# Kernel optimization log

Measured on AMD Instinct MI355X. Metric: run time of the kernel, lower is better.

The kernel has to match this reference:

```python
import jax, jax.numpy as jnp
from jax import lax
import numpy as np

N = 10000   # nodes
E = 160000  # edges (avg degree 16)
C = 64      # in_channels / out_channels
T = 12      # input time steps
H = 64      # hidden_channels (must be 64 for GReTo psi broadcast)
TS = T - 2  # tlen_spconv after first causal conv (k=3, no padding)
F = H * TS  # GCN feature dim = 640

def _conv1d(x, w, b):
    # x: [N, Cin, T], w: [Cout, Cin, K] -> [N, Cout, T-K+1] (causal, no padding)
    out = lax.conv_general_dilated(x, w, window_strides=(1,), padding='VALID',
                                   dimension_numbers=('NCH', 'OIH', 'NCH'))
    return out + b[None, :, None]

def _time_conv(x, w1, b1, w2, b2):
    # gated TCN: tanh(conv1) * sigmoid(conv2)
    return jnp.tanh(_conv1d(x, w1, b1)) * jax.nn.sigmoid(_conv1d(x, w2, b2))

def _gcn(x, W, b, src, dst, ew, n):
    # PyG GCNConv: add self-loops (weight 1.0), symmetric normalization, x@W, scatter-sum, +bias
    loop = jnp.arange(n)
    s = jnp.concatenate([src, loop])
    d = jnp.concatenate([dst, loop])
    w = jnp.concatenate([ew, jnp.ones((n,), ew.dtype)])
    deg = jax.ops.segment_sum(w, d, num_segments=n)
    dis = jnp.where(deg > 0, deg ** -0.5, 0.0)
    norm = dis[s] * w * dis[d]                 # [E+N]
    h = x @ W                                  # [n, F]
    out = jax.ops.segment_sum(norm[:, None] * h[s], d, num_segments=n)
    return out + b

def setup_inputs():
    key = jax.random.key(0)
    ks = jax.random.split(key, 16)
    s = 0.05
    return {
        'x': jax.random.normal(ks[0], (N, C, T), jnp.float32),
        'edge_index': jax.random.randint(ks[1], (2, E), 0, N),
        'edge_attr': jax.random.uniform(ks[2], (E, 2), dtype=jnp.float32),
        'ND_t': jax.random.normal(ks[3], (N, 3), jnp.float32),
        'tc1_w1': jax.random.normal(ks[4], (H, C, 3), jnp.float32) * s,
        'tc1_b1': jnp.zeros((H,), jnp.float32),
        'tc1_w2': jax.random.normal(ks[5], (H, C, 3), jnp.float32) * s,
        'tc1_b2': jnp.zeros((H,), jnp.float32),
        'W_pos': jax.random.normal(ks[6], (F, F), jnp.float32) * s,
        'b_pos': jnp.zeros((F,), jnp.float32),
        'W_neg': jax.random.normal(ks[7], (F, F), jnp.float32) * s,
        'b_neg': jnp.zeros((F,), jnp.float32),
        'gre_W': jax.random.normal(ks[8], (2 * H, H), jnp.float32) * s,
        'gre_b': jnp.zeros((H,), jnp.float32),
        'psi_W1': jax.random.normal(ks[9], (3, 64), jnp.float32) * s,
        'psi_b1': jnp.zeros((64,), jnp.float32),
        'psi_W2': jax.random.normal(ks[10], (64, 3), jnp.float32) * s,
        'psi_b2': jnp.zeros((3,), jnp.float32),
        'tc2_w1': jax.random.normal(ks[11], (C, H, 3), jnp.float32) * s,
        'tc2_b1': jnp.zeros((C,), jnp.float32),
        'tc2_w2': jax.random.normal(ks[12], (C, H, 3), jnp.float32) * s,
        'tc2_b2': jnp.zeros((C,), jnp.float32),
    }

def reference(x, edge_index, edge_attr, ND_t,
              tc1_w1, tc1_b1, tc1_w2, tc1_b2,
              W_pos, b_pos, W_neg, b_neg, gre_W, gre_b,
              psi_W1, psi_b1, psi_W2, psi_b2,
              tc2_w1, tc2_b1, tc2_w2, tc2_b2):
    n = x.shape[0]
    out1 = _time_conv(x, tc1_w1, tc1_b1, tc1_w2, tc1_b2)   # [N, H, TS]
    d0, d1, d2 = out1.shape
    src, dst = edge_index[0], edge_index[1]
    w_pos = edge_attr[:, 0] + 1.0
    w_neg = edge_attr[:, 1] + 1.0
    # psi: [N, 3] -> one scalar per node per hop; repeat_interleave in torch is
    # just a broadcast since psi is constant over the H and TS dims
    psi = jax.nn.relu(ND_t @ psi_W1 + psi_b1) @ psi_W2 + psi_b2
    out0 = out1.reshape(d0, -1)                             # [N, H*TS]
    cur = out0
    acc = jnp.zeros((d0, d1, d2), x.dtype)
    for i in range(3):  # k = 3 positive-graph hops
        h = jax.nn.relu(_gcn(cur, W_pos, b_pos, src, dst, w_pos, n).reshape(d0, d1, d2))
        acc = acc + psi[:, i][:, None, None] * h
        cur = h.reshape(d0, -1)
    out_neg = jax.nn.relu(_gcn(out0, W_neg, b_neg, src, dst, w_neg, n).reshape(d0, d1, d2))
    out2 = jnp.concatenate([acc, out_neg], axis=1)          # [N, 2H, TS]
    out2 = jax.nn.relu(jnp.einsum('nct,cd->ndt', out2, gre_W) + gre_b[None, :, None])
    out3 = _time_conv(out2, tc2_w1, tc2_b1, tc2_w2, tc2_b2) # [N, C, TS-2]
    return out3
```

## Files before the change

kernel.cpp:

```cpp
#include <hip/hip_runtime.h>
#include <math.h>

#define NN   10000
#define NE   160000
#define CCH  64
#define TIN  12
#define HCH  64
#define TSP  10
#define FF   640
#define TOUT 8
#define NR   (NN * TSP)
#define NR2  (NN * TOUT)


typedef _Float16 f16;
typedef _Float16 f16x4 __attribute__((ext_vector_type(4)));
typedef _Float16 f16x8 __attribute__((ext_vector_type(8)));
typedef float f32x4 __attribute__((ext_vector_type(4)));

#define GLD_LDS(gsrc, ldst) __builtin_amdgcn_global_load_lds( \
    (const __attribute__((address_space(1))) void*)(gsrc),    \
    (__attribute__((address_space(3))) void*)(ldst), 16, 0, 0)

__global__ __launch_bounds__(256) void k_xT(const float* __restrict__ x, f16* __restrict__ xT)
{
    __shared__ float xs[4][CCH * TIN];
    int node0 = blockIdx.x * 4;
    for (int i = threadIdx.x; i < 4 * CCH * TIN; i += 256) {
        int nn = i / (CCH * TIN), off = i % (CCH * TIN);
        int g = node0 + nn;
        xs[nn][off] = (g < NN) ? x[(size_t)g * CCH * TIN + off] : 0.f;
    }
    __syncthreads();
    for (int i = threadIdx.x; i < 4 * CCH * TIN; i += 256) {
        int nn = i / (CCH * TIN), off = i % (CCH * TIN);
        int t = off >> 6, c = off & 63;
        int g = node0 + nn;
        if (g < NN) xT[(size_t)g * (CCH * TIN) + off] = (f16)xs[nn][c * TIN + t];
    }
}

__global__ void k_wconv2(const float* __restrict__ w1a, const float* __restrict__ w2a,
                         const float* __restrict__ w1b, const float* __restrict__ w2b,
                         f16* __restrict__ d1, f16* __restrict__ d2)
{
    int tid = blockIdx.x * 256 + threadIdx.x;
    const int half = 128 * 192;
    if (tid >= 2 * half) return;
    int which = tid / half, r = tid % half;
    const float* s1 = which ? w1b : w1a;
    const float* s2 = which ? w2b : w2a;
    f16* dst = which ? d2 : d1;
    int o = r / 192, j = r % 192;
    int k = j >> 6, ci = j & 63;
    const float* src = (o < 64) ? s1 : s2;
    dst[r] = (f16)src[((o & 63) * 64 + ci) * 3 + k];
}

__global__ __launch_bounds__(256) void k_tcn1g(const f16* __restrict__ A,
                                               const f16* __restrict__ Bw,
                                               const float* __restrict__ b1,
                                               const float* __restrict__ b2,
                                               f16* __restrict__ out)
{
    __shared__ f16 Bs[128][200];
    int tid = threadIdx.x;
#pragma unroll
    for (int i = 0; i < 12; ++i) {
        int c = tid + i * 256;
        int row = c / 24, seg = (c % 24) * 8;
        *(f16x8*)&Bs[row][seg] = *(const f16x8*)&Bw[row * 192 + seg];
    }
    __syncthreads();

    int w = tid >> 6, l = tid & 63;
    int row0 = blockIdx.x * 128 + w * 32;
    int lrow = l & 15, lk = (l >> 4) * 8;

    size_t abase[2];
#pragma unroll
    for (int m = 0; m < 2; ++m) {
        int rr = row0 + m * 16 + lrow;
        int rc = (rr < NR) ? rr : NR - 1;
        int n = rc / 10, t = rc - n * 10;
        abase[m] = (size_t)n * 768 + t * 64 + lk;
    }
    f32x4 acc[2][8];
#pragma unroll
    for (int m = 0; m < 2; ++m)
#pragma unroll
        for (int n = 0; n < 8; ++n)
            acc[m][n] = (f32x4){0.f, 0.f, 0.f, 0.f};

#pragma unroll
    for (int ks = 0; ks < 6; ++ks) {
        f16x8 af[2], bf[8];
#pragma unroll
        for (int m = 0; m < 2; ++m)
            af[m] = *(const f16x8*)&A[abase[m] + ks * 32];
#pragma unroll
        for (int n = 0; n < 8; ++n)
            bf[n] = *(const f16x8*)&Bs[n * 16 + lrow][ks * 32 + lk];
#pragma unroll
        for (int m = 0; m < 2; ++m)
#pragma unroll
            for (int n = 0; n < 8; ++n)
                acc[m][n] = __builtin_amdgcn_mfma_f32_16x16x32_f16(af[m], bf[n], acc[m][n], 0, 0, 0);
    }
    int og = (l >> 4) * 4;
#pragma unroll
    for (int m = 0; m < 2; ++m) {
#pragma unroll
        for (int n = 0; n < 4; ++n) {
            int h = n * 16 + lrow;
            float bb1 = b1[h], bb2 = b2[h];
#pragma unroll
            for (int rr = 0; rr < 4; ++rr) {
                int R = row0 + m * 16 + og + rr;
                if (R < NR) {
                    float g1 = acc[m][n][rr] + bb1;
                    float g2 = acc[m][n + 4][rr] + bb2;
                    float e = __expf(2.f * g1);
                    float th = 1.f - 2.f / (e + 1.f);
                    float sg = 1.f / (1.f + __expf(-g2));
                    out[(size_t)R * 64 + h] = (f16)(th * sg);
                }
            }
        }
    }
}

__global__ __launch_bounds__(256) void k_tcn2g(const f16* __restrict__ A,
                                               const f16* __restrict__ Bw,
                                               const float* __restrict__ b1,
                                               const float* __restrict__ b2,
                                               float* __restrict__ out)
{
    __shared__ f16 Bs[128][200];
    int tid = threadIdx.x;
#pragma unroll
    for (int i = 0; i < 12; ++i) {
        int c = tid + i * 256;
        int row = c / 24, seg = (c % 24) * 8;
        *(f16x8*)&Bs[row][seg] = *(const f16x8*)&Bw[row * 192 + seg];
    }
    __syncthreads();

    int w = tid >> 6, l = tid & 63;
    int row0 = blockIdx.x * 128 + w * 32;
    int lrow = l & 15, lk = (l >> 4) * 8;

    size_t abase[2];
#pragma unroll
    for (int m = 0; m < 2; ++m) {
        int rr = row0 + m * 16 + lrow;
        int rc = (rr < NR2) ? rr : NR2 - 1;
        int n = rc >> 3, t = rc & 7;
        abase[m] = (size_t)n * FF + t * 64 + lk;
    }
    f32x4 acc[2][8];
#pragma unroll
    for (int m = 0; m < 2; ++m)
#pragma unroll
        for (int n = 0; n < 8; ++n)
            acc[m][n] = (f32x4){0.f, 0.f, 0.f, 0.f};

#pragma unroll
    for (int ks = 0; ks < 6; ++ks) {
        f16x8 af[2], bf[8];
#pragma unroll
        for (int m = 0; m < 2; ++m)
            af[m] = *(const f16x8*)&A[abase[m] + ks * 32];
#pragma unroll
        for (int n = 0; n < 8; ++n)
            bf[n] = *(const f16x8*)&Bs[n * 16 + lrow][ks * 32 + lk];
#pragma unroll
        for (int m = 0; m < 2; ++m)
#pragma unroll
            for (int n = 0; n < 8; ++n)
                acc[m][n] = __builtin_amdgcn_mfma_f32_16x16x32_f16(af[m], bf[n], acc[m][n], 0, 0, 0);
    }
    int og = (l >> 4) * 4;
#pragma unroll
    for (int m = 0; m < 2; ++m) {
#pragma unroll
        for (int n = 0; n < 4; ++n) {
            int c = n * 16 + lrow;
            float bb1 = b1[c], bb2 = b2[c];
#pragma unroll
            for (int rr = 0; rr < 4; ++rr) {
                int R = row0 + m * 16 + og + rr;
                if (R < NR2) {
                    float g1 = acc[m][n][rr] + bb1;
                    float g2 = acc[m][n + 4][rr] + bb2;
                    float e = __expf(2.f * g1);
                    float th = 1.f - 2.f / (e + 1.f);
                    float sg = 1.f / (1.f + __expf(-g2));
                    int n2 = R >> 3, t2 = R & 7;
                    out[(size_t)n2 * (CCH * TOUT) + c * TOUT + t2] = th * sg;
                }
            }
        }
    }
}

__global__ void k_psi(const float* __restrict__ ND, const float* __restrict__ W1,
                      const float* __restrict__ b1, const float* __restrict__ W2,
                      const float* __restrict__ b2, float* __restrict__ psi)
{
    int n = blockIdx.x * blockDim.x + threadIdx.x;
    if (n >= NN) return;
    float d0 = ND[n * 3], d1 = ND[n * 3 + 1], d2 = ND[n * 3 + 2];
    float o0 = b2[0], o1 = b2[1], o2 = b2[2];
    for (int j = 0; j < 64; ++j) {
        float hv = d0 * W1[j] + d1 * W1[64 + j] + d2 * W1[128 + j] + b1[j];
        hv = fmaxf(hv, 0.f);
        o0 += hv * W2[j * 3 + 0];
        o1 += hv * W2[j * 3 + 1];
        o2 += hv * W2[j * 3 + 2];
    }
    psi[n * 3 + 0] = o0; psi[n * 3 + 1] = o1; psi[n * 3 + 2] = o2;
}

__global__ void k_deg(const int* __restrict__ ei, const float* __restrict__ ea,
                      int* __restrict__ cnt, float* __restrict__ degp, float* __restrict__ degn)
{
    int e = blockIdx.x * blockDim.x + threadIdx.x;
    if (e >= NE) return;
    int d = ei[NE + e];
    atomicAdd(&cnt[d], 1);
    atomicAdd(&degp[d], ea[e * 2 + 0] + 1.f);
    atomicAdd(&degn[d], ea[e * 2 + 1] + 1.f);
}

__global__ void k_dis(const float* __restrict__ degp, const float* __restrict__ degn,
                      float* __restrict__ disp, float* __restrict__ disn)
{
    int n = blockIdx.x * blockDim.x + threadIdx.x;
    if (n >= NN) return;
    disp[n] = 1.f / sqrtf(degp[n] + 1.f);
    disn[n] = 1.f / sqrtf(degn[n] + 1.f);
}

__global__ __launch_bounds__(1024) void k_scan(const int* __restrict__ cnt, int* __restrict__ rowptr)
{
    __shared__ int buf[1024];
    __shared__ int carry;
    if (threadIdx.x == 0) carry = 0;
    __syncthreads();
    for (int base = 0; base < NN; base += 1024) {
        int i = base + threadIdx.x;
        int v = (i < NN) ? cnt[i] : 0;
        buf[threadIdx.x] = v;
        __syncthreads();
        for (int off = 1; off < 1024; off <<= 1) {
            int t = (threadIdx.x >= (unsigned)off) ? buf[threadIdx.x - off] : 0;
            __syncthreads();
            buf[threadIdx.x] += t;
            __syncthreads();
        }
        if (i < NN) rowptr[i] = carry + buf[threadIdx.x] - v;
        __syncthreads();
        if (threadIdx.x == 0) carry += buf[1023];
        __syncthreads();
    }
    if (threadIdx.x == 0) rowptr[NN] = carry;
}

__global__ void k_fill(const int* __restrict__ ei, const float* __restrict__ ea,
                       const int* __restrict__ rowptr, int* __restrict__ cursor,
                       const float* __restrict__ disp, const float* __restrict__ disn,
                       int* __restrict__ colsrc, float* __restrict__ normp, float* __restrict__ normn)
{
    int e = blockIdx.x * blockDim.x + threadIdx.x;
    if (e >= NE) return;
    int s = ei[e], d = ei[NE + e];
    int slot = atomicAdd(&cursor[d], 1);
    int idx = rowptr[d] + slot;
    colsrc[idx] = s;
    normp[idx] = disp[s] * (ea[e * 2 + 0] + 1.f) * disp[d];
    normn[idx] = disn[s] * (ea[e * 2 + 1] + 1.f) * disn[d];
}

__global__ __launch_bounds__(256) void k_wsplit2(const float* __restrict__ Wa,
                                                 const float* __restrict__ Wb,
                                                 f16* __restrict__ Wt)
{
    __shared__ float t[32][33];
    const float* W = blockIdx.z ? Wb : Wa;
    f16* dst = Wt + (size_t)blockIdx.z * FF * FF;
    int bx = blockIdx.x * 32;
    int by = blockIdx.y * 32;
    int tx = threadIdx.x & 31, ty = threadIdx.x >> 5;
#pragma unroll
    for (int j = 0; j < 4; ++j)
        t[ty + j * 8][tx] = W[(size_t)(bx + ty + j * 8) * 640 + by + tx];
    __syncthreads();
#pragma unroll
    for (int j = 0; j < 4; ++j)
        dst[(size_t)(by + ty + j * 8) * 640 + bx + tx] = (f16)t[tx][ty + j * 8];
}

__global__ __launch_bounds__(640) void k_perm2(const f16* __restrict__ Wt0,
                                               f16* __restrict__ Wp, f16* __restrict__ Wn)
{
    __shared__ f16 row[FF];
    const f16* src = Wt0 + (size_t)blockIdx.z * FF * FF;
    f16* dst = blockIdx.z ? Wn : Wp;
    int np = blockIdx.x;
    int n = (np & 63) * 10 + (np >> 6);
    int tid = threadIdx.x;
    row[tid] = src[(size_t)n * FF + tid];
    __syncthreads();
    int k = (tid & 63) * 10 + (tid >> 6);
    dst[(size_t)np * FF + tid] = row[k];
}

__global__ void k_gwt(const float* __restrict__ gW, f16* __restrict__ gWt)
{
    int tid = blockIdx.x * 256 + threadIdx.x;
    if (tid >= 128 * 64) return;
    int c = tid >> 6, d = tid & 63;
    gWt[d * 128 + c] = (f16)gW[tid];
}

__global__ __launch_bounds__(256) void k_gemm16(const f16* __restrict__ A,
                                                const f16* __restrict__ Bt,
                                                f16* __restrict__ C, int M)
{
    __shared__ f16 As[128 * 32];
    __shared__ f16 Bs[64 * 32];
    int tid = threadIdx.x;
    int row0 = blockIdx.y * 128;
    int col0 = blockIdx.x * 64;
    int w = tid >> 6, l = tid & 63;
    int wr = (w >> 1) * 64;
    int wc = (w & 1) * 32;
    int lrow = l & 15;
    int lk = (l >> 4) * 8;

    int arow = w * 32 + (l >> 2);
    int brow = w * 16 + (l >> 2);
    int seg  = (l & 3) * 8;

    f32x4 acc[4][2];
#pragma unroll
    for (int m = 0; m < 4; ++m)
#pragma unroll
        for (int n = 0; n < 2; ++n)
            acc[m][n] = (f32x4){0.f, 0.f, 0.f, 0.f};

    for (int k0 = 0; k0 < FF; k0 += 32) {
        __syncthreads();
        GLD_LDS(&A[(size_t)(row0 + arow) * FF + k0 + seg],       &As[w * 1024]);
        GLD_LDS(&A[(size_t)(row0 + arow + 16) * FF + k0 + seg],  &As[w * 1024 + 512]);
        GLD_LDS(&Bt[(size_t)(col0 + brow) * FF + k0 + seg],      &Bs[w * 512]);
        __syncthreads();
        f16x8 af[4], bf[2];
#pragma unroll
        for (int m = 0; m < 4; ++m)
            af[m] = *(const f16x8*)&As[(wr + m * 16 + lrow) * 32 + lk];
#pragma unroll
        for (int n = 0; n < 2; ++n)
            bf[n] = *(const f16x8*)&Bs[(wc + n * 16 + lrow) * 32 + lk];
#pragma unroll
        for (int m = 0; m < 4; ++m)
#pragma unroll
            for (int n = 0; n < 2; ++n)
                acc[m][n] = __builtin_amdgcn_mfma_f32_16x16x32_f16(af[m], bf[n], acc[m][n], 0, 0, 0);
    }
    int orow = (l >> 4) * 4;
#pragma unroll
    for (int m = 0; m < 4; ++m) {
#pragma unroll
        for (int r = 0; r < 4; ++r) {
            int rr = row0 + wr + m * 16 + orow + r;
            if (rr < M) {
#pragma unroll
                for (int n = 0; n < 2; ++n)
                    C[(size_t)rr * FF + col0 + wc + n * 16 + lrow] = (f16)acc[m][n][r];
            }
        }
    }
}

__global__ __launch_bounds__(192) void k_agg(const f16* __restrict__ hsrc,
                      const int* __restrict__ rowptr, const int* __restrict__ colsrc,
                      const float* __restrict__ enorm, const float* __restrict__ dis,
                      const float* __restrict__ bias, f16* __restrict__ hout)
{
    __shared__ int   s_idx[128];
    __shared__ float s_w[128];
    int d = blockIdx.x;
    int lane = threadIdx.x;
    int c0 = lane * 4;
    bool act = lane < 160;
    float v0 = 0.f, v1 = 0.f, v2 = 0.f, v3 = 0.f;
    if (act) {
        float selfw = dis[d] * dis[d];
        f16x4 self = *(const f16x4*)&hsrc[(size_t)d * FF + c0];
        v0 = selfw * (float)self[0];
        v1 = selfw * (float)self[1];
        v2 = selfw * (float)self[2];
        v3 = selfw * (float)self[3];
    }
    int beg = rowptr[d], end = rowptr[d + 1];
    for (int base = beg; base < end; base += 128) {
        int cnt = (end - base < 128) ? (end - base) : 128;
        __syncthreads();
        for (int j = lane; j < cnt; j += 192) {
            s_idx[j] = colsrc[base + j];
            s_w[j]   = enorm[base + j];
        }
        __syncthreads();
        if (act) {
            for (int i = 0; i < cnt; ++i) {
                f16x4 p = *(const f16x4*)&hsrc[(size_t)s_idx[i] * FF + c0];
                float w = s_w[i];
                v0 += w * (float)p[0];
                v1 += w * (float)p[1];
                v2 += w * (float)p[2];
                v3 += w * (float)p[3];
            }
        }
    }
    if (act) {
        f16x4 o;
        float vv[4] = {v0, v1, v2, v3};
#pragma unroll
        for (int j = 0; j < 4; ++j) {
            int c = c0 + j;
            o[j] = (f16)fmaxf(vv[j] + bias[(c & 63) * 10 + (c >> 6)], 0.f);
        }
        *(f16x4*)&hout[(size_t)d * FF + c0] = o;
    }
}

__global__ __launch_bounds__(256) void k_greto2(const f16* __restrict__ h1,
                        const f16* __restrict__ h2, const f16* __restrict__ h3,
                        const f16* __restrict__ hneg, const float* __restrict__ psi,
                        const f16* __restrict__ gWt, const float* __restrict__ gb,
                        f16* __restrict__ out)
{
    __shared__ f16 As[128][132];
    __shared__ f16 Bs[64][132];
    int tid = threadIdx.x;
    int row0 = blockIdx.x * 128;

    for (int cb = tid; cb < 1024; cb += 256) {
        int d = cb >> 4, seg = (cb & 15) * 8;
        *(f16x8*)&Bs[d][seg] = *(const f16x8*)&gWt[d * 128 + seg];
    }
    int lr = tid >> 1, side = tid & 1;
    int r = row0 + lr;
    if (r < NR) {
        int n = r / 10, t = r - (r / 10) * 10;
        size_t base = (size_t)n * FF + t * 64;
        if (side == 0) {
            float p0 = psi[n * 3], p1 = psi[n * 3 + 1], p2 = psi[n * 3 + 2];
#pragma unroll
            for (int i = 0; i < 8; ++i) {
                f16x8 a = *(const f16x8*)&h1[base + i * 8];
                f16x8 b = *(const f16x8*)&h2[base + i * 8];
                f16x8 c = *(const f16x8*)&h3[base + i * 8];
                f16x8 o;
#pragma unroll
                for (int j = 0; j < 8; ++j)
                    o[j] = (f16)(p0 * (float)a[j] + p1 * (float)b[j] + p2 * (float)c[j]);
                *(f16x8*)&As[lr][i * 8] = o;
            }
        } else {
#pragma unroll
            for (int i = 0; i < 8; ++i)
                *(f16x8*)&As[lr][64 + i * 8] = *(const f16x8*)&hneg[base + i * 8];
        }
    } else {
        f16x8 z = {};
#pragma unroll
        for (int i = 0; i < 8; ++i)
            *(f16x8*)&As[lr][side * 64 + i * 8] = z;
    }
    __syncthreads();

    int w = tid >> 6, l = tid & 63;
    int wr = w * 32;
    int lrow = l & 15;
    int lk = (l >> 4) * 8;
    f32x4 acc[2][4];
#pragma unroll
    for (int m = 0; m < 2; ++m)
#pragma unroll
        for (int n = 0; n < 4; ++n)
            acc[m][n] = (f32x4){0.f, 0.f, 0.f, 0.f};
#pragma unroll
    for (int ks = 0; ks < 4; ++ks) {
        f16x8 af[2], bf[4];
#pragma unroll
        for (int m = 0; m < 2; ++m)
            af[m] = *(const f16x8*)&As[wr + m * 16 + lrow][ks * 32 + lk];
#pragma unroll
        for (int n = 0; n < 4; ++n)
            bf[n] = *(const f16x8*)&Bs[n * 16 + lrow][ks * 32 + lk];
#pragma unroll
        for (int m = 0; m < 2; ++m)
#pragma unroll
            for (int n = 0; n < 4; ++n)
                acc[m][n] = __builtin_amdgcn_mfma_f32_16x16x32_f16(af[m], bf[n], acc[m][n], 0, 0, 0);
    }
    int orow = (l >> 4) * 4;
#pragma unroll
    for (int m = 0; m < 2; ++m) {
#pragma unroll
        for (int rr = 0; rr < 4; ++rr) {
            int ro = row0 + wr + m * 16 + orow + rr;
            if (ro < NR) {
#pragma unroll
                for (int n = 0; n < 4; ++n) {
                    int col = n * 16 + lrow;
                    out[(size_t)ro * 64 + col] = (f16)fmaxf(acc[m][n][rr] + gb[col], 0.f);
                }
            }
        }
    }
}

extern "C" void kernel_launch(void* const* d_in, const int* in_sizes, int n_in,
                              void* d_out, int out_size, void* d_ws, size_t ws_size,
                              hipStream_t stream)
{
    const float* x     = (const float*)d_in[0];
    const int*   ei    = (const int*)  d_in[1];
    const float* ea    = (const float*)d_in[2];
    const float* ndt   = (const float*)d_in[3];
    const float* tc1w1 = (const float*)d_in[4];
    const float* tc1b1 = (const float*)d_in[5];
    const float* tc1w2 = (const float*)d_in[6];
    const float* tc1b2 = (const float*)d_in[7];
    const float* Wpos  = (const float*)d_in[8];
    const float* bpos  = (const float*)d_in[9];
    const float* Wneg  = (const float*)d_in[10];
    const float* bneg  = (const float*)d_in[11];
    const float* greW  = (const float*)d_in[12];
    const float* greb  = (const float*)d_in[13];
    const float* psiW1 = (const float*)d_in[14];
    const float* psib1 = (const float*)d_in[15];
    const float* psiW2 = (const float*)d_in[16];
    const float* psib2 = (const float*)d_in[17];
    const float* tc2w1 = (const float*)d_in[18];
    const float* tc2b1 = (const float*)d_in[19];
    const float* tc2w2 = (const float*)d_in[20];
    const float* tc2b2 = (const float*)d_in[21];
    float* out = (float*)d_out;

    char* p = (char*)d_ws;
    int*   cnt   = (int*)p;   p += (size_t)NN * 4;
    int*   cursor= (int*)p;   p += (size_t)NN * 4;
    float* degp  = (float*)p; p += (size_t)NN * 4;
    float* degn  = (float*)p; p += (size_t)NN * 4;
    f16*   xT    = (f16*)p;   p += (size_t)NN * CCH * TIN * 2;
    f16*   out0h = (f16*)p;   p += (size_t)NN * FF * 2;
    f16*   h1    = (f16*)p;   p += (size_t)NN * FF * 2;
    f16*   h2    = (f16*)p;   p += (size_t)NN * FF * 2;
    f16*   h3    = (f16*)p;   p += (size_t)NN * FF * 2;
    f16*   hneg  = (f16*)p;   p += (size_t)NN * FF * 2;
    f16*   Cb16  = (f16*)p;   p += (size_t)NN * FF * 2;
    f16*   Gbuf  = (f16*)p;   p += (size_t)NN * FF * 2;
    f16*   Wtp   = (f16*)p;   p += (size_t)FF * FF * 2;
    f16*   Wtn   = (f16*)p;   p += (size_t)FF * FF * 2;
    f16*   Wtmp  = (f16*)p;   p += (size_t)2 * FF * FF * 2;
    f16*   gWt   = (f16*)p;   p += (size_t)128 * 64 * 2;
    f16*   Bw1   = (f16*)p;   p += (size_t)128 * 192 * 2;
    f16*   Bw2   = (f16*)p;   p += (size_t)128 * 192 * 2;
    float* psib  = (float*)p; p += (size_t)NN * 3 * 4;
    float* disp  = (float*)p; p += (size_t)NN * 4;
    float* disn  = (float*)p; p += (size_t)NN * 4;
    float* normp = (float*)p; p += (size_t)NE * 4;
    float* normn = (float*)p; p += (size_t)NE * 4;
    int* rowptr  = (int*)p;   p += (size_t)(NN + 1) * 4;
    int* colsrc  = (int*)p;   p += (size_t)NE * 4;

    (void)hipMemsetAsync(cnt, 0, (size_t)4 * NN * 4, stream);

    k_xT<<<2500, 256, 0, stream>>>(x, xT);
    k_wconv2<<<(2 * 128 * 192 + 255) / 256, 256, 0, stream>>>(tc1w1, tc1w2, tc2w1, tc2w2, Bw1, Bw2);
    k_tcn1g<<<(NR + 127) / 128, 256, 0, stream>>>(xT, Bw1, tc1b1, tc1b2, out0h);
    k_psi<<<(NN + 255) / 256, 256, 0, stream>>>(ndt, psiW1, psib1, psiW2, psib2, psib);
    k_deg<<<(NE + 255) / 256, 256, 0, stream>>>(ei, ea, cnt, degp, degn);
    k_dis<<<(NN + 255) / 256, 256, 0, stream>>>(degp, degn, disp, disn);
    k_scan<<<1, 1024, 0, stream>>>(cnt, rowptr);
    k_fill<<<(NE + 255) / 256, 256, 0, stream>>>(ei, ea, rowptr, cursor, disp, disn,
                                                 colsrc, normp, normn);
    dim3 wgrid(20, 20, 2);
    k_wsplit2<<<wgrid, 256, 0, stream>>>(Wpos, Wneg, Wtmp);
    dim3 pgrid(FF, 1, 2);
    k_perm2<<<pgrid, 640, 0, stream>>>(Wtmp, Wtp, Wtn);
    k_gwt<<<(128 * 64 + 255) / 256, 256, 0, stream>>>(greW, gWt);

    dim3 ggrid(FF / 64, (NN + 127) / 128);
    k_gemm16<<<ggrid, 256, 0, stream>>>(out0h, Wtp, Cb16, NN);
    k_agg<<<NN, 192, 0, stream>>>(Cb16, rowptr, colsrc, normp, disp, bpos, h1);
    k_gemm16<<<ggrid, 256, 0, stream>>>(h1, Wtp, Cb16, NN);
    k_agg<<<NN, 192, 0, stream>>>(Cb16, rowptr, colsrc, normp, disp, bpos, h2);
    k_gemm16<<<ggrid, 256, 0, stream>>>(h2, Wtp, Cb16, NN);
    k_agg<<<NN, 192, 0, stream>>>(Cb16, rowptr, colsrc, normp, disp, bpos, h3);
    k_gemm16<<<ggrid, 256, 0, stream>>>(out0h, Wtn, Cb16, NN);
    k_agg<<<NN, 192, 0, stream>>>(Cb16, rowptr, colsrc, normn, disn, bneg, hneg);
    k_greto2<<<(NR + 127) / 128, 256, 0, stream>>>(h1, h2, h3, hneg, psib, gWt, greb, Gbuf);
    k_tcn2g<<<(NR2 + 127) / 128, 256, 0, stream>>>(Gbuf, Bw2, tc2b1, tc2b2, out);
}
```

Before: 397.2 us.

## Merge preprocessing kernels, parallelize scan, widen aggregation to 8-wide vectors

Folds the x transpose, conv weight conversion, psi MLP, GReTo weight transpose, degree counting and W split-transpose into one block-indexed prep kernel. This cuts the number of launches. The degree-inverse-sqrt step moves into the scan kernel, and the scan becomes a single pass where each thread sums 10 counts before one block-wide prefix sum. The GCN aggregation kernel now uses 128 threads with 8-element f16 vector loads per lane instead of 192 threads with 4-element loads, which halves the gather instructions per neighbor row but leaves fewer active lanes per node.

```diff
diff --git a/kernel.cpp b/kernel.cpp
--- a/kernel.cpp
+++ b/kernel.cpp
@@ -12,9 +12,7 @@
 #define NR   (NN * TSP)
 #define NR2  (NN * TOUT)
 
-
 typedef _Float16 f16;
-typedef _Float16 f16x4 __attribute__((ext_vector_type(4)));
 typedef _Float16 f16x8 __attribute__((ext_vector_type(8)));
 typedef float f32x4 __attribute__((ext_vector_type(4)));
 
@@ -22,39 +20,104 @@
     (const __attribute__((address_space(1))) void*)(gsrc),    \
     (__attribute__((address_space(3))) void*)(ldst), 16, 0, 0)
 
-__global__ __launch_bounds__(256) void k_xT(const float* __restrict__ x, f16* __restrict__ xT)
-{
-    __shared__ float xs[4][CCH * TIN];
-    int node0 = blockIdx.x * 4;
-    for (int i = threadIdx.x; i < 4 * CCH * TIN; i += 256) {
-        int nn = i / (CCH * TIN), off = i % (CCH * TIN);
-        int g = node0 + nn;
-        xs[nn][off] = (g < NN) ? x[(size_t)g * CCH * TIN + off] : 0.f;
-    }
-    __syncthreads();
-    for (int i = threadIdx.x; i < 4 * CCH * TIN; i += 256) {
-        int nn = i / (CCH * TIN), off = i % (CCH * TIN);
-        int t = off >> 6, c = off & 63;
-        int g = node0 + nn;
-        if (g < NN) xT[(size_t)g * (CCH * TIN) + off] = (f16)xs[nn][c * TIN + t];
-    }
-}
-
-__global__ void k_wconv2(const float* __restrict__ w1a, const float* __restrict__ w2a,
-                         const float* __restrict__ w1b, const float* __restrict__ w2b,
-                         f16* __restrict__ d1, f16* __restrict__ d2)
-{
-    int tid = blockIdx.x * 256 + threadIdx.x;
-    const int half = 128 * 192;
-    if (tid >= 2 * half) return;
-    int which = tid / half, r = tid % half;
-    const float* s1 = which ? w1b : w1a;
-    const float* s2 = which ? w2b : w2a;
-    f16* dst = which ? d2 : d1;
-    int o = r / 192, j = r % 192;
-    int k = j >> 6, ci = j & 63;
-    const float* src = (o < 64) ? s1 : s2;
-    dst[r] = (f16)src[((o & 63) * 64 + ci) * 3 + k];
+#define PB_XT   2500
+#define PB_WC   (PB_XT + 192)
+#define PB_PSI  (PB_WC + 40)
+#define PB_GWT  (PB_PSI + 32)
+#define PB_DEG  (PB_GWT + 625)
+#define PB_WS   (PB_DEG + 800)
+
+__global__ __launch_bounds__(256) void k_prep(
+    const float* __restrict__ x, f16* __restrict__ xT,
+    const float* __restrict__ tc1w1, const float* __restrict__ tc1w2,
+    const float* __restrict__ tc2w1, const float* __restrict__ tc2w2,
+    f16* __restrict__ Bw1, f16* __restrict__ Bw2,
+    const float* __restrict__ ND, const float* __restrict__ pW1,
+    const float* __restrict__ pb1, const float* __restrict__ pW2,
+    const float* __restrict__ pb2, float* __restrict__ psi,
+    const float* __restrict__ gW, f16* __restrict__ gWt,
+    const int* __restrict__ ei, const float* __restrict__ ea,
+    int* __restrict__ cnt, float* __restrict__ degp, float* __restrict__ degn,
+    const float* __restrict__ Wpos, const float* __restrict__ Wneg,
+    f16* __restrict__ Wtmp)
+{
+    __shared__ float smem[3072];
+    int blk = blockIdx.x;
+    int tid = threadIdx.x;
+
+    if (blk < PB_XT) {
+        float (*xs)[CCH * TIN] = (float(*)[CCH * TIN])smem;
+        int node0 = blk * 4;
+        for (int i = tid; i < 4 * CCH * TIN; i += 256) {
+            int nn = i / (CCH * TIN), off = i % (CCH * TIN);
+            int g = node0 + nn;
+            xs[nn][off] = (g < NN) ? x[(size_t)g * CCH * TIN + off] : 0.f;
+        }
+        __syncthreads();
+        for (int i = tid; i < 4 * CCH * TIN; i += 256) {
+            int nn = i / (CCH * TIN), off = i % (CCH * TIN);
+            int t = off >> 6, c = off & 63;
+            int g = node0 + nn;
+            if (g < NN) xT[(size_t)g * (CCH * TIN) + off] = (f16)xs[nn][c * TIN + t];
+        }
+    } else if (blk < PB_WC) {
+        int t2 = (blk - PB_XT) * 256 + tid;
+        const int half = 128 * 192;
+        if (t2 < 2 * half) {
+            int which = t2 / half, r = t2 % half;
+            const float* s1 = which ? tc2w1 : tc1w1;
+            const float* s2 = which ? tc2w2 : tc1w2;
+            f16* dst = which ? Bw2 : Bw1;
+            int o = r / 192, j = r % 192;
+            int k = j >> 6, ci = j & 63;
+            const float* src = (o < 64) ? s1 : s2;
+            dst[r] = (f16)src[((o & 63) * 64 + ci) * 3 + k];
+        }
+    } else if (blk < PB_PSI) {
+        int n = (blk - PB_WC) * 256 + tid;
+        if (n < NN) {
+            float d0 = ND[n * 3], d1 = ND[n * 3 + 1], d2 = ND[n * 3 + 2];
+            float o0 = pb2[0], o1 = pb2[1], o2 = pb2[2];
+            for (int j = 0; j < 64; ++j) {
+                float hv = d0 * pW1[j] + d1 * pW1[64 + j] + d2 * pW1[128 + j] + pb1[j];
+                hv = fmaxf(hv, 0.f);
+                o0 += hv * pW2[j * 3 + 0];
+                o1 += hv * pW2[j * 3 + 1];
+                o2 += hv * pW2[j * 3 + 2];
+            }
+            psi[n * 3 + 0] = o0; psi[n * 3 + 1] = o1; psi[n * 3 + 2] = o2;
+        }
+    } else if (blk < PB_GWT) {
+        int t2 = (blk - PB_PSI) * 256 + tid;
+        if (t2 < 128 * 64) {
+            int c = t2 >> 6, d = t2 & 63;
+            gWt[d * 128 + c] = (f16)gW[t2];
+        }
+    } else if (blk < PB_DEG) {
+        int e = (blk - PB_GWT) * 256 + tid;
+        if (e < NE) {
+            int d = ei[NE + e];
+            atomicAdd(&cnt[d], 1);
+            atomicAdd(&degp[d], ea[e * 2 + 0] + 1.f);
+            atomicAdd(&degn[d], ea[e * 2 + 1] + 1.f);
+        }
+    } else {
+        float (*tt)[33] = (float(*)[33])smem;
+        int rel = blk - PB_DEG;
+        int z = rel / 400, r2 = rel % 400;
+        const float* W = z ? Wneg : Wpos;
+        f16* dst = Wtmp + (size_t)z * FF * FF;
+        int bx = (r2 / 20) * 32;
+        int by = (r2 % 20) * 32;
+        int tx = tid & 31, ty = tid >> 5;
+#pragma unroll
+        for (int j = 0; j < 4; ++j)
+            tt[ty + j * 8][tx] = W[(size_t)(bx + ty + j * 8) * 640 + by + tx];
+        __syncthreads();
+#pragma unroll
+        for (int j = 0; j < 4; ++j)
+            dst[(size_t)(by + ty + j * 8) * 640 + bx + tx] = (f16)tt[tx][ty + j * 8];
+    }
 }
 
 __global__ __launch_bounds__(256) void k_tcn1g(const f16* __restrict__ A,
@@ -204,67 +267,38 @@
     }
 }
 
-__global__ void k_psi(const float* __restrict__ ND, const float* __restrict__ W1,
-                      const float* __restrict__ b1, const float* __restrict__ W2,
-                      const float* __restrict__ b2, float* __restrict__ psi)
-{
-    int n = blockIdx.x * blockDim.x + threadIdx.x;
-    if (n >= NN) return;
-    float d0 = ND[n * 3], d1 = ND[n * 3 + 1], d2 = ND[n * 3 + 2];
-    float o0 = b2[0], o1 = b2[1], o2 = b2[2];
-    for (int j = 0; j < 64; ++j) {
-        float hv = d0 * W1[j] + d1 * W1[64 + j] + d2 * W1[128 + j] + b1[j];
-        hv = fmaxf(hv, 0.f);
-        o0 += hv * W2[j * 3 + 0];
-        o1 += hv * W2[j * 3 + 1];
-        o2 += hv * W2[j * 3 + 2];
-    }
-    psi[n * 3 + 0] = o0; psi[n * 3 + 1] = o1; psi[n * 3 + 2] = o2;
-}
-
-__global__ void k_deg(const int* __restrict__ ei, const float* __restrict__ ea,
-                      int* __restrict__ cnt, float* __restrict__ degp, float* __restrict__ degn)
-{
-    int e = blockIdx.x * blockDim.x + threadIdx.x;
-    if (e >= NE) return;
-    int d = ei[NE + e];
-    atomicAdd(&cnt[d], 1);
-    atomicAdd(&degp[d], ea[e * 2 + 0] + 1.f);
-    atomicAdd(&degn[d], ea[e * 2 + 1] + 1.f);
-}
-
-__global__ void k_dis(const float* __restrict__ degp, const float* __restrict__ degn,
+__global__ __launch_bounds__(1024) void k_scan(const int* __restrict__ cnt,
+                      int* __restrict__ rowptr,
+                      const float* __restrict__ degp, const float* __restrict__ degn,
                       float* __restrict__ disp, float* __restrict__ disn)
 {
-    int n = blockIdx.x * blockDim.x + threadIdx.x;
-    if (n >= NN) return;
-    disp[n] = 1.f / sqrtf(degp[n] + 1.f);
-    disn[n] = 1.f / sqrtf(degn[n] + 1.f);
-}
-
-__global__ __launch_bounds__(1024) void k_scan(const int* __restrict__ cnt, int* __restrict__ rowptr)
-{
-    __shared__ int buf[1024];
-    __shared__ int carry;
-    if (threadIdx.x == 0) carry = 0;
+    int tid = threadIdx.x;
+    for (int i = tid; i < NN; i += 1024) {
+        disp[i] = 1.f / sqrtf(degp[i] + 1.f);
+        disn[i] = 1.f / sqrtf(degn[i] + 1.f);
+    }
+    __shared__ int part[1024];
+    int base = tid * 10;
+    int loc[10];
+    int sum = 0;
+    if (tid < 1000) {
+#pragma unroll
+        for (int j = 0; j < 10; ++j) { loc[j] = sum; sum += cnt[base + j]; }
+    }
+    part[tid] = (tid < 1000) ? sum : 0;
     __syncthreads();
-    for (int base = 0; base < NN; base += 1024) {
-        int i = base + threadIdx.x;
-        int v = (i < NN) ? cnt[i] : 0;
-        buf[threadIdx.x] = v;
-        __syncthreads();
-        for (int off = 1; off < 1024; off <<= 1) {
-            int t = (threadIdx.x >= (unsigned)off) ? buf[threadIdx.x - off] : 0;
-            __syncthreads();
-            buf[threadIdx.x] += t;
-            __syncthreads();
-        }
-        if (i < NN) rowptr[i] = carry + buf[threadIdx.x] - v;
-        __syncthreads();
-        if (threadIdx.x == 0) carry += buf[1023];
-        __syncthreads();
-    }
-    if (threadIdx.x == 0) rowptr[NN] = carry;
+    for (int off = 1; off < 1024; off <<= 1) {
+        int t = (tid >= off) ? part[tid - off] : 0;
+        __syncthreads();
+        part[tid] += t;
+        __syncthreads();
+    }
+    int prefix = (tid > 0) ? part[tid - 1] : 0;
+    if (tid < 1000) {
+#pragma unroll
+        for (int j = 0; j < 10; ++j) rowptr[base + j] = prefix + loc[j];
+    }
+    if (tid == 0) rowptr[NN] = part[1023];
 }
 
 __global__ void k_fill(const int* __restrict__ ei, const float* __restrict__ ea,
@@ -280,25 +314,6 @@
     colsrc[idx] = s;
     normp[idx] = disp[s] * (ea[e * 2 + 0] + 1.f) * disp[d];
     normn[idx] = disn[s] * (ea[e * 2 + 1] + 1.f) * disn[d];
-}
-
-__global__ __launch_bounds__(256) void k_wsplit2(const float* __restrict__ Wa,
-                                                 const float* __restrict__ Wb,
-                                                 f16* __restrict__ Wt)
-{
-    __shared__ float t[32][33];
-    const float* W = blockIdx.z ? Wb : Wa;
-    f16* dst = Wt + (size_t)blockIdx.z * FF * FF;
-    int bx = blockIdx.x * 32;
-    int by = blockIdx.y * 32;
-    int tx = threadIdx.x & 31, ty = threadIdx.x >> 5;
-#pragma unroll
-    for (int j = 0; j < 4; ++j)
-        t[ty + j * 8][tx] = W[(size_t)(bx + ty + j * 8) * 640 + by + tx];
-    __syncthreads();
-#pragma unroll
-    for (int j = 0; j < 4; ++j)
-        dst[(size_t)(by + ty + j * 8) * 640 + bx + tx] = (f16)t[tx][ty + j * 8];
 }
 
 __global__ __launch_bounds__(640) void k_perm2(const f16* __restrict__ Wt0,
@@ -316,14 +331,6 @@
     dst[(size_t)np * FF + tid] = row[k];
 }
 
-__global__ void k_gwt(const float* __restrict__ gW, f16* __restrict__ gWt)
-{
-    int tid = blockIdx.x * 256 + threadIdx.x;
-    if (tid >= 128 * 64) return;
-    int c = tid >> 6, d = tid & 63;
-    gWt[d * 128 + c] = (f16)gW[tid];
-}
-
 __global__ __launch_bounds__(256) void k_gemm16(const f16* __restrict__ A,
                                                 const f16* __restrict__ Bt,
                                                 f16* __restrict__ C, int M)
@@ -384,7 +391,7 @@
     }
 }
 
-__global__ __launch_bounds__(192) void k_agg(const f16* __restrict__ hsrc,
+__global__ __launch_bounds__(128) void k_agg(const f16* __restrict__ hsrc,
                       const int* __restrict__ rowptr, const int* __restrict__ colsrc,
                       const float* __restrict__ enorm, const float* __restrict__ dis,
                       const float* __restrict__ bias, f16* __restrict__ hout)
@@ -393,46 +400,41 @@
     __shared__ float s_w[128];
     int d = blockIdx.x;
     int lane = threadIdx.x;
-    int c0 = lane * 4;
-    bool act = lane < 160;
-    float v0 = 0.f, v1 = 0.f, v2 = 0.f, v3 = 0.f;
+    int c0 = lane * 8;
+    bool act = lane < 80;
+    float v[8] = {0.f, 0.f, 0.f, 0.f, 0.f, 0.f, 0.f, 0.f};
     if (act) {
         float selfw = dis[d] * dis[d];
-        f16x4 self = *(const f16x4*)&hsrc[(size_t)d * FF + c0];
-        v0 = selfw * (float)self[0];
-        v1 = selfw * (float)self[1];
-        v2 = selfw * (float)self[2];
-        v3 = selfw * (float)self[3];
+        f16x8 self = *(const f16x8*)&hsrc[(size_t)d * FF + c0];
+#pragma unroll
+        for (int j = 0; j < 8; ++j) v[j] = selfw * (float)self[j];
     }
     int beg = rowptr[d], end = rowptr[d + 1];
     for (int base = beg; base < end; base += 128) {
         int cnt = (end - base < 128) ? (end - base) : 128;
         __syncthreads();
-        for (int j = lane; j < cnt; j += 192) {
-            s_idx[j] = colsrc[base + j];
-            s_w[j]   = enorm[base + j];
+        if (lane < cnt) {
+            s_idx[lane] = colsrc[base + lane];
+            s_w[lane]   = enorm[base + lane];
         }
         __syncthreads();
         if (act) {
             for (int i = 0; i < cnt; ++i) {
-                f16x4 p = *(const f16x4*)&hsrc[(size_t)s_idx[i] * FF + c0];
+                f16x8 p = *(const f16x8*)&hsrc[(size_t)s_idx[i] * FF + c0];
                 float w = s_w[i];
-                v0 += w * (float)p[0];
-                v1 += w * (float)p[1];
-                v2 += w * (float)p[2];
-                v3 += w * (float)p[3];
+#pragma unroll
+                for (int j = 0; j < 8; ++j) v[j] += w * (float)p[j];
             }
         }
     }
     if (act) {
-        f16x4 o;
-        float vv[4] = {v0, v1, v2, v3};
-#pragma unroll
-        for (int j = 0; j < 4; ++j) {
+        f16x8 o;
+#pragma unroll
+        for (int j = 0; j < 8; ++j) {
             int c = c0 + j;
-            o[j] = (f16)fmaxf(vv[j] + bias[(c & 63) * 10 + (c >> 6)], 0.f);
-        }
-        *(f16x4*)&hout[(size_t)d * FF + c0] = o;
+            o[j] = (f16)fmaxf(v[j] + bias[(c & 63) * 10 + (c >> 6)], 0.f);
+        }
+        *(f16x8*)&hout[(size_t)d * FF + c0] = o;
     }
 }
 
@@ -581,30 +583,26 @@
 
     (void)hipMemsetAsync(cnt, 0, (size_t)4 * NN * 4, stream);
 
-    k_xT<<<2500, 256, 0, stream>>>(x, xT);
-    k_wconv2<<<(2 * 128 * 192 + 255) / 256, 256, 0, stream>>>(tc1w1, tc1w2, tc2w1, tc2w2, Bw1, Bw2);
-    k_tcn1g<<<(NR + 127) / 128, 256, 0, stream>>>(xT, Bw1, tc1b1, tc1b2, out0h);
-    k_psi<<<(NN + 255) / 256, 256, 0, stream>>>(ndt, psiW1, psib1, psiW2, psib2, psib);
-    k_deg<<<(NE + 255) / 256, 256, 0, stream>>>(ei, ea, cnt, degp, degn);
-    k_dis<<<(NN + 255) / 256, 256, 0, stream>>>(degp, degn, disp, disn);
-    k_scan<<<1, 1024, 0, stream>>>(cnt, rowptr);
+    k_prep<<<PB_WS, 256, 0, stream>>>(x, xT, tc1w1, tc1w2, tc2w1, tc2w2, Bw1, Bw2,
+                                      ndt, psiW1, psib1, psiW2, psib2, psib,
+                                      greW, gWt, ei, ea, cnt, degp, degn,
+                                      Wpos, Wneg, Wtmp);
+    k_scan<<<1, 1024, 0, stream>>>(cnt, rowptr, degp, degn, disp, disn);
     k_fill<<<(NE + 255) / 256, 256, 0, stream>>>(ei, ea, rowptr, cursor, disp, disn,
                                                  colsrc, normp, normn);
-    dim3 wgrid(20, 20, 2);
-    k_wsplit2<<<wgrid, 256, 0, stream>>>(Wpos, Wneg, Wtmp);
     dim3 pgrid(FF, 1, 2);
     k_perm2<<<pgrid, 640, 0, stream>>>(Wtmp, Wtp, Wtn);
-    k_gwt<<<(128 * 64 + 255) / 256, 256, 0, stream>>>(greW, gWt);
+    k_tcn1g<<<(NR + 127) / 128, 256, 0, stream>>>(xT, Bw1, tc1b1, tc1b2, out0h);
 
     dim3 ggrid(FF / 64, (NN + 127) / 128);
     k_gemm16<<<ggrid, 256, 0, stream>>>(out0h, Wtp, Cb16, NN);
-    k_agg<<<NN, 192, 0, stream>>>(Cb16, rowptr, colsrc, normp, disp, bpos, h1);
+    k_agg<<<NN, 128, 0, stream>>>(Cb16, rowptr, colsrc, normp, disp, bpos, h1);
     k_gemm16<<<ggrid, 256, 0, stream>>>(h1, Wtp, Cb16, NN);
-    k_agg<<<NN, 192, 0, stream>>>(Cb16, rowptr, colsrc, normp, disp, bpos, h2);
+    k_agg<<<NN, 128, 0, stream>>>(Cb16, rowptr, colsrc, normp, disp, bpos, h2);
     k_gemm16<<<ggrid, 256, 0, stream>>>(h2, Wtp, Cb16, NN);
-    k_agg<<<NN, 192, 0, stream>>>(Cb16, rowptr, colsrc, normp, disp, bpos, h3);
+    k_agg<<<NN, 128, 0, stream>>>(Cb16, rowptr, colsrc, normp, disp, bpos, h3);
     k_gemm16<<<ggrid, 256, 0, stream>>>(out0h, Wtn, Cb16, NN);
-    k_agg<<<NN, 192, 0, stream>>>(Cb16, rowptr, colsrc, normn, disn, bneg, hneg);
+    k_agg<<<NN, 128, 0, stream>>>(Cb16, rowptr, colsrc, normn, disn, bneg, hneg);
     k_greto2<<<(NR + 127) / 128, 256, 0, stream>>>(h1, h2, h3, hneg, psib, gWt, greb, Gbuf);
     k_tcn2g<<<(NR2 + 127) / 128, 256, 0, stream>>>(Gbuf, Bw2, tc2b1, tc2b2, out);
 }
```

Result: faster. 346.4 us (-12.8%).
